# Performance work log

Measured on AMD Instinct MI355X. Metric: run time of the kernel, lower is better.

The kernel has to match this reference:

```python
import jax, jax.numpy as jnp
import numpy as np

N = 200_000           # particles
E = 6_400_000         # neighbor pairs (~32 per particle)
SUPPORT = 0.05
EPS = SUPPORT ** 2 * 0.1
DELTA = 0.1
C0 = 10.0 * float(np.sqrt(2.0 * 9.81 * 0.3))
REST_DENSITY = 1000.0
_KC = 7.0 / float(np.pi)  # 2D Wendland C2 normalization


def kernel_gradient(q, dirs, h):
    # Wendland C2 (2D): W = C/h^2 (1-q)^4 (1+4q), q = r/h in [0,1]
    # dW/dr = C/h^3 * (-20 q (1-q)^3), directed along unit vector dirs
    dkdq = -20.0 * q * (1.0 - q) ** 3 * _KC
    return dirs * (dkdq / h ** 3)[:, None]


def setup_inputs() -> dict:
    key = jax.random.key(0)
    k = jax.random.split(key, 7)
    i = jnp.sort(jax.random.randint(k[0], (E,), 0, N))
    j = jax.random.randint(k[1], (E,), 0, N)
    fluidPosition = jax.random.uniform(k[2], (N, 2), dtype=jnp.float32)
    dx2 = (SUPPORT * 0.5) ** 2
    fluidVolume = dx2 * (1.0 + 0.01 * jax.random.normal(k[3], (N,), dtype=jnp.float32))
    fluidDensity = 0.95 + 0.1 * jax.random.uniform(k[4], (N,), dtype=jnp.float32)
    d = jax.random.normal(k[5], (E, 2), dtype=jnp.float32)
    distances = d / (jnp.linalg.norm(d, axis=1, keepdims=True) + 1e-8)  # unit directions
    radialDistances = jax.random.uniform(k[6], (E,), dtype=jnp.float32, minval=0.05, maxval=1.0)
    return {"fluidPosition": fluidPosition, "fluidVolume": fluidVolume,
            "fluidDensity": fluidDensity, "distances": distances,
            "radialDistances": radialDistances, "i": i, "j": j}


def reference(fluidPosition, fluidVolume, fluidDensity, distances, radialDistances, i, j):
    h = SUPPORT
    n = fluidDensity.shape[0]
    gradW = kernel_gradient(radialDistances, distances, h)          # [E,2]
    r_ba = -distances * (radialDistances * h)[:, None]              # [E,2] displacement
    Vj = fluidVolume[j]

    # --- normalization matrix: sum_j 2 Vj * outer(r_ba, gradW) ---
    term = jnp.einsum('nu,nv->nuv', r_ba, gradW) * (2.0 * Vj)[:, None, None]
    M = jax.ops.segment_sum(term, i, num_segments=n)                # [N,2,2]

    # --- pseudo-inverse + renormalized kernel gradient per edge ---
    Li = jnp.linalg.pinv(M)                                         # [N,2,2]
    grad = jnp.einsum('nuv,nv->nu', Li[i], gradW)                   # [E,2]
    dwij_mag = jnp.sum(jnp.abs(gradW), axis=1)                      # L1 norms
    norm_mag = jnp.sum(jnp.abs(grad), axis=1)
    change = jnp.abs(norm_mag - dwij_mag) / (dwij_mag + 1e-4 * h)
    grad = jnp.where((change < 0.1)[:, None], grad, gradW)

    # --- renormalized density gradient ---
    rho = fluidDensity * REST_DENSITY
    rho_ba = rho[j] - rho[i]
    gradRho = jax.ops.segment_sum((2.0 * rho_ba * Vj)[:, None] * grad, i, num_segments=n)

    # --- deltaSPH density diffusion ---
    rji2 = jnp.sum(r_ba * r_ba, axis=1) + EPS
    densityTerm = 0.5 * jnp.einsum('nu,nu->n', gradRho[i] + gradRho[j], r_ba)
    gradTerm = jnp.einsum('nu,nu->n', gradW, r_ba / rji2[:, None])
    prod = (rho_ba + densityTerm) * gradTerm
    return 2.0 * h * DELTA * C0 * jax.ops.segment_sum(prod * Vj, i, num_segments=n)
```

## Files before the change

kernel.cpp:

```cpp
#include <hip/hip_runtime.h>
#include <hip/hip_fp16.h>
#include <math.h>

#define WAVE   64
#define NPB    32
#define BLOCKT 256
#define SMAX   2

#define KC        2.2281692032865347f
#define H         0.05f
#define INV_H2    400.0f
#define INV_H3    8000.0f
#define EPS_REF   0.00025f
#define K_OUT     0.24261080f
#define REST_RHO  1000.0f

__device__ __forceinline__ float wendland_dkdq(float q) {
    float o = 1.f - q;
    return -20.f * q * o * o * o * KC;
}

union H2F { __half2 h; float f; };
__device__ __forceinline__ float   h2_as_f(__half2 h) { H2F u; u.h = h; return u.f; }
__device__ __forceinline__ __half2 f_as_h2(float f)   { H2F u; u.f = f; return u.h; }

template<int NV>
__device__ __forceinline__ void seg_reduce4(const int k[4], float v[4][NV], float* base) {
    const int lane = threadIdx.x & (WAVE - 1);
    const int k0 = k[0], k3 = k[3];
    const bool split = (k0 != k3);
    const int firstLen  = (k[1]==k0) ? ((k[2]==k0) ? ((k[3]==k0)?4:3) : 2) : 1;
    const int lastStart = (k[2]==k3) ? ((k[1]==k3) ? ((k[0]==k3)?0:1) : 2) : 3;

    float vin[NV], vfirst[NV];
#pragma unroll
    for (int c = 0; c < NV; ++c) {
        float s = v[3][c];
        if (lastStart <= 2) s += v[2][c];
        if (lastStart <= 1) s += v[1][c];
        if (lastStart == 0) s += v[0][c];
        vin[c] = s;
        float f = v[0][c];
        if (firstLen >= 2) f += v[1][c];
        if (firstLen >= 3) f += v[2][c];
        if (firstLen >= 4) f += v[3][c];
        vfirst[c] = f;
    }
#pragma unroll
    for (int idx = 1; idx <= 2; ++idx) {
        if (idx >= firstLen && idx < lastStart && k[idx] >= 0) {
#pragma unroll
            for (int c = 0; c < NV; ++c)
                atomicAdd(base + (size_t)k[idx] * NV + c, v[idx][c]);
        }
    }
    float S[NV];
#pragma unroll
    for (int c = 0; c < NV; ++c) S[c] = vin[c];
    const int klast = k3;
#pragma unroll
    for (int d = 1; d <= 16; d <<= 1) {
        int okey = __shfl_up(klast, d, WAVE);
        float ov[NV];
#pragma unroll
        for (int c = 0; c < NV; ++c) ov[c] = __shfl_up(S[c], d, WAVE);
        if (lane >= d && okey == klast) {
#pragma unroll
            for (int c = 0; c < NV; ++c) S[c] += ov[c];
        }
    }
    const int prevk = __shfl_up(klast, 1, WAVE);
    float P[NV];
#pragma unroll
    for (int c = 0; c < NV; ++c) P[c] = __shfl_up(S[c], 1, WAVE);
    if (split && k0 >= 0) {
        const bool carry = (lane > 0 && prevk == k0);
#pragma unroll
        for (int c = 0; c < NV; ++c)
            atomicAdd(base + (size_t)k0 * NV + c, vfirst[c] + (carry ? P[c] : 0.f));
    }
    const int nk0 = __shfl_down(k0, 1, WAVE);
    const bool tail = (lane == WAVE - 1) || (nk0 != klast);
    if (tail && klast >= 0) {
#pragma unroll
        for (int c = 0; c < NV; ++c)
            atomicAdd(base + (size_t)klast * NV + c, S[c]);
    }
}

struct EW { int jv[4]; float qv[4], dxv[4], dyv[4]; int kv[4]; bool okv[4]; };

__device__ __forceinline__ void load_win(long e0, int beg, int end, int E,
        const int* __restrict__ ej, const float* __restrict__ qarr,
        const float2* __restrict__ dirs, const unsigned char* __restrict__ key8,
        EW& w) {
    if (e0 + 3 < (long)E) {
        int4   j4 = *(const int4*)(ej + e0);
        float4 q4 = *(const float4*)(qarr + e0);
        float4 dA = *(const float4*)((const float*)dirs + 2 * e0);
        float4 dB = *(const float4*)((const float*)dirs + 2 * e0 + 4);
        uchar4 kk = *(const uchar4*)(key8 + e0);
        w.jv[0]=j4.x; w.jv[1]=j4.y; w.jv[2]=j4.z; w.jv[3]=j4.w;
        w.qv[0]=q4.x; w.qv[1]=q4.y; w.qv[2]=q4.z; w.qv[3]=q4.w;
        w.dxv[0]=dA.x; w.dyv[0]=dA.y; w.dxv[1]=dA.z; w.dyv[1]=dA.w;
        w.dxv[2]=dB.x; w.dyv[2]=dB.y; w.dxv[3]=dB.z; w.dyv[3]=dB.w;
        w.kv[0]=kk.x; w.kv[1]=kk.y; w.kv[2]=kk.z; w.kv[3]=kk.w;
    } else {
#pragma unroll
        for (int u = 0; u < 4; ++u) {
            long e = e0 + u;
            if (e < (long)E) {
                w.jv[u] = ej[e]; w.qv[u] = qarr[e]; w.kv[u] = key8[e];
                float2 d = dirs[e]; w.dxv[u] = d.x; w.dyv[u] = d.y;
            } else { w.jv[u]=0; w.qv[u]=0.f; w.dxv[u]=0.f; w.dyv[u]=0.f; w.kv[u]=0; }
        }
    }
#pragma unroll
    for (int u = 0; u < 4; ++u) {
        long e = e0 + u;
        w.okv[u] = (e >= (long)beg) && (e < (long)end);
    }
}

__global__ void k_prep(const int* __restrict__ ei, const float* __restrict__ vol,
                       const float* __restrict__ dens, int* __restrict__ rowptr,
                       float2* __restrict__ vd, unsigned char* __restrict__ key8,
                       int N, int E) {
    int e = blockIdx.x * blockDim.x + threadIdx.x;
    if (e <= E) {
        int prev = (e == 0) ? -1 : ei[e - 1];
        int cur  = (e == E) ? N  : ei[e];
        for (int t = prev + 1; t <= cur; ++t) rowptr[t] = e;
        if (e < E) key8[e] = (unsigned char)(cur & (NPB - 1));
    }
    if (e < N) vd[e] = make_float2(vol[e], dens[e]);
}

__global__ __launch_bounds__(BLOCKT, 4)
void k_AC(const int* __restrict__ ej, const float* __restrict__ qarr,
          const float2* __restrict__ dirs, const float2* __restrict__ vd,
          const int* __restrict__ rowptr, const unsigned char* __restrict__ key8,
          __half2* __restrict__ cst,
          float2* __restrict__ g2, float* __restrict__ outp, int N, int E) {
    __shared__ float  acc6[NPB * 6];
    __shared__ float  Lild[NPB * 3];
    __shared__ float  gld[NPB * 2];
    __shared__ float2 vdl[NPB];
    const int tid = threadIdx.x;
    const int n0  = blockIdx.x * NPB;
    const int nHi = min(n0 + NPB, N);
    if (tid < NPB && n0 + tid < N) vdl[tid] = vd[n0 + tid];
    if (tid < NPB * 6) acc6[tid] = 0.f;
    if (tid < NPB * 2) gld[tid] = 0.f;
    __syncthreads();
    const int  beg = rowptr[n0], end = rowptr[nHi];
    const long beg4 = (long)beg & ~3L;
    const int  waveBase = tid & ~(WAVE - 1);

    int   li_s[4 * SMAX];
    float gwx_s[4 * SMAX], gwy_s[4 * SMAX], val_s[4 * SMAX];
#pragma unroll
    for (int x = 0; x < 4 * SMAX; ++x) { li_s[x] = -1; gwx_s[x]=gwy_s[x]=val_s[x]=0.f; }

#pragma unroll
    for (int c = 0; c < SMAX; ++c) {
        long ebw = beg4 + ((long)c * BLOCKT + waveBase) * 4;
        if (ebw < (long)end) {
            long e0 = beg4 + ((long)c * BLOCKT + tid) * 4;
            EW wd; load_win(e0, beg, end, E, ej, qarr, dirs, key8, wd);
            const bool all4 = wd.okv[0] && wd.okv[1] && wd.okv[2] && wd.okv[3];
            float4 cpack;
            int k[4]; float v[4][6];
#pragma unroll
            for (int u = 0; u < 4; ++u) {
                k[u] = -1;
#pragma unroll
                for (int c2 = 0; c2 < 6; ++c2) v[u][c2] = 0.f;
                if (wd.okv[u]) {
                    int li = wd.kv[u];
                    float q = wd.qv[u], dx = wd.dxv[u], dy = wd.dyv[u];
                    float2 vdj = vd[wd.jv[u]];
                    float wq = wendland_dkdq(q);
                    float t  = q * wq * INV_H2;
                    float s  = -2.f * vdj.x * t;
                    float w2 = wq * INV_H3;
                    float gwx = dx * w2, gwy = dy * w2;
                    float rx = -dx * q * H, ry = -dy * q * H;
                    float rji2 = rx * rx + ry * ry + EPS_REF;
                    float gT = -t / rji2;
                    float gv = gT * vdj.x;
                    float rho_ba = REST_RHO * (vdj.y - vdl[li].y);
                    k[u] = li;
                    v[u][0] = s * dx * dx; v[u][1] = s * dx * dy; v[u][2] = s * dy * dy;
                    v[u][3] = rho_ba * gv; v[u][4] = rx * gv;    v[u][5] = ry * gv;
                    __half2 cp = __floats2half2_rn(0.5f * rx * gv, 0.5f * ry * gv);
                    if (all4) (&cpack.x)[u] = h2_as_f(cp);
                    else      cst[e0 + u] = cp;
                    li_s[c*4+u] = li; gwx_s[c*4+u] = gwx; gwy_s[c*4+u] = gwy;
                    val_s[c*4+u] = 2.f * rho_ba * vdj.x;
                }
            }
            if (all4) ((float4*)cst)[e0 >> 2] = cpack;
            seg_reduce4<6>(k, v, acc6);
        }
    }
    for (int c = SMAX; ; ++c) {
        long ebw = beg4 + ((long)c * BLOCKT + waveBase) * 4;
        if (ebw >= (long)end) break;
        long e0 = beg4 + ((long)c * BLOCKT + tid) * 4;
        EW wd; load_win(e0, beg, end, E, ej, qarr, dirs, key8, wd);
        int k[4]; float v[4][6];
#pragma unroll
        for (int u = 0; u < 4; ++u) {
            k[u] = -1;
#pragma unroll
            for (int c2 = 0; c2 < 6; ++c2) v[u][c2] = 0.f;
            if (wd.okv[u]) {
                int li = wd.kv[u];
                float q = wd.qv[u], dx = wd.dxv[u], dy = wd.dyv[u];
                float2 vdj = vd[wd.jv[u]];
                float wq = wendland_dkdq(q);
                float t  = q * wq * INV_H2;
                float s  = -2.f * vdj.x * t;
                float w2 = wq * INV_H3;
                float gwx = dx * w2, gwy = dy * w2;
                float rx = -dx * q * H, ry = -dy * q * H;
                float rji2 = rx * rx + ry * ry + EPS_REF;
                float gT = -t / rji2;
                float gv = gT * vdj.x;
                float rho_ba = REST_RHO * (vdj.y - vdl[li].y);
                k[u] = li;
                v[u][0] = s * dx * dx; v[u][1] = s * dx * dy; v[u][2] = s * dy * dy;
                v[u][3] = rho_ba * gv; v[u][4] = rx * gv;    v[u][5] = ry * gv;
                cst[e0 + u] = __floats2half2_rn(0.5f * rx * gv, 0.5f * ry * gv);
            }
        }
        seg_reduce4<6>(k, v, acc6);
    }
    __syncthreads();

    if (tid < NPB) {
        float a = acc6[6*tid], b = acc6[6*tid+1], cc = acc6[6*tid+2];
        float half_tr   = 0.5f * (a + cc);
        float half_diff = 0.5f * (a - cc);
        float disc = sqrtf(half_diff * half_diff + b * b);
        float l1 = half_tr + disc, l2 = half_tr - disc;
        float smax = fmaxf(fabsf(l1), fabsf(l2));
        float cutoff = 2.3841858e-6f * smax;
        float i00 = 0.f, i01 = 0.f, i11 = 0.f;
        if (fabsf(l2) > cutoff) {
            float inv = 1.0f / (a * cc - b * b);
            i00 =  cc * inv; i01 = -b * inv; i11 = a * inv;
        } else if (fabsf(l1) > cutoff) {
            float vax = b,       vay = l1 - a;
            float vbx = l1 - cc, vby = b;
            float na = vax*vax + vay*vay, nb = vbx*vbx + vby*vby;
            float vx, vy, n2;
            if (nb >= na) { vx = vbx; vy = vby; n2 = nb; }
            else          { vx = vax; vy = vay; n2 = na; }
            float inv = 1.0f / (l1 * n2);
            i00 = vx*vx*inv; i01 = vx*vy*inv; i11 = vy*vy*inv;
        }
        Lild[3*tid] = i00; Lild[3*tid+1] = i01; Lild[3*tid+2] = i11;
    }
    __syncthreads();

#pragma unroll
    for (int c = 0; c < SMAX; ++c) {
        long ebw = beg4 + ((long)c * BLOCKT + waveBase) * 4;
        if (ebw < (long)end) {
            int k[4]; float v[4][2];
#pragma unroll
            for (int u = 0; u < 4; ++u) {
                int li = li_s[c*4+u];
                k[u] = li; v[u][0] = v[u][1] = 0.f;
                if (li >= 0) {
                    float gwx = gwx_s[c*4+u], gwy = gwy_s[c*4+u];
                    float L0 = Lild[3*li], L1 = Lild[3*li+1], L2v = Lild[3*li+2];
                    float gx = L0 * gwx + L1 * gwy;
                    float gy = L1 * gwx + L2v * gwy;
                    float dm = fabsf(gwx) + fabsf(gwy);
                    float nm = fabsf(gx) + fabsf(gy);
                    float change = fabsf(nm - dm) / (dm + 1e-4f * H);
                    if (!(change < 0.1f)) { gx = gwx; gy = gwy; }
                    v[u][0] = val_s[c*4+u] * gx;
                    v[u][1] = val_s[c*4+u] * gy;
                }
            }
            seg_reduce4<2>(k, v, gld);
        }
    }
    for (int c = SMAX; ; ++c) {
        long ebw = beg4 + ((long)c * BLOCKT + waveBase) * 4;
        if (ebw >= (long)end) break;
        long e0 = beg4 + ((long)c * BLOCKT + tid) * 4;
        EW wd; load_win(e0, beg, end, E, ej, qarr, dirs, key8, wd);
        int k[4]; float v[4][2];
#pragma unroll
        for (int u = 0; u < 4; ++u) {
            k[u] = -1; v[u][0] = v[u][1] = 0.f;
            if (wd.okv[u]) {
                int li = wd.kv[u];
                float q = wd.qv[u], dx = wd.dxv[u], dy = wd.dyv[u];
                float2 vdj = vd[wd.jv[u]];
                float w2 = wendland_dkdq(q) * INV_H3;
                float gwx = dx * w2, gwy = dy * w2;
                float L0 = Lild[3*li], L1 = Lild[3*li+1], L2v = Lild[3*li+2];
                float gx = L0 * gwx + L1 * gwy;
                float gy = L1 * gwx + L2v * gwy;
                float dm = fabsf(gwx) + fabsf(gwy);
                float nm = fabsf(gx) + fabsf(gy);
                float change = fabsf(nm - dm) / (dm + 1e-4f * H);
                if (!(change < 0.1f)) { gx = gwx; gy = gwy; }
                float val = 2.f * REST_RHO * (vdj.y - vdl[li].y) * vdj.x;
                k[u] = li; v[u][0] = val * gx; v[u][1] = val * gy;
            }
        }
        seg_reduce4<2>(k, v, gld);
    }
    __syncthreads();
    if (tid < NPB && n0 + tid < N) {
        float gx = gld[2*tid], gy = gld[2*tid+1];
        g2[n0 + tid]   = make_float2(gx, gy);
        outp[n0 + tid] = acc6[6*tid+3] + 0.5f * (gx * acc6[6*tid+4] + gy * acc6[6*tid+5]);
    }
}

__global__ __launch_bounds__(BLOCKT, 4)
void k_D(const int* __restrict__ ej, const unsigned char* __restrict__ key8,
         const __half2* __restrict__ cst,
         const float2* __restrict__ g2, const float* __restrict__ outp,
         const int* __restrict__ rowptr, float* __restrict__ out, int N, int E) {
    __shared__ float outl[NPB];
    const int tid = threadIdx.x;
    const int n0  = blockIdx.x * NPB;
    const int nHi = min(n0 + NPB, N);
    if (tid < NPB) outl[tid] = 0.f;
    __syncthreads();
    const int  beg = rowptr[n0], end = rowptr[nHi];
    const long beg4 = (long)beg & ~3L;
    const int  waveBase = tid & ~(WAVE - 1);

    for (int c = 0; ; ++c) {
        long ebw = beg4 + ((long)c * BLOCKT + waveBase) * 4;
        if (ebw >= (long)end) break;
        long e0 = beg4 + ((long)c * BLOCKT + tid) * 4;
        int jv[4], kv[4]; float cv[4]; bool okv[4];
        if (e0 + 3 < (long)E) {
            int4   j4 = *(const int4*)(ej + e0);
            float4 c4 = ((const float4*)cst)[e0 >> 2];
            uchar4 kk = *(const uchar4*)(key8 + e0);
            jv[0]=j4.x; jv[1]=j4.y; jv[2]=j4.z; jv[3]=j4.w;
            cv[0]=c4.x; cv[1]=c4.y; cv[2]=c4.z; cv[3]=c4.w;
            kv[0]=kk.x; kv[1]=kk.y; kv[2]=kk.z; kv[3]=kk.w;
        } else {
#pragma unroll
            for (int u = 0; u < 4; ++u) {
                long e = e0 + u;
                if (e < (long)E) { jv[u] = ej[e]; cv[u] = h2_as_f(cst[e]); kv[u] = key8[e]; }
                else             { jv[u] = 0;     cv[u] = 0.f;             kv[u] = 0; }
            }
        }
#pragma unroll
        for (int u = 0; u < 4; ++u) {
            long e = e0 + u;
            okv[u] = (e >= (long)beg) && (e < (long)end);
        }
        float2 gj4[4];
#pragma unroll
        for (int u = 0; u < 4; ++u)
            gj4[u] = okv[u] ? g2[jv[u]] : make_float2(0.f, 0.f);
        int k[4]; float v[4][1];
#pragma unroll
        for (int u = 0; u < 4; ++u) {
            k[u] = -1; v[u][0] = 0.f;
            if (okv[u]) {
                __half2 ch = f_as_h2(cv[u]);
                k[u] = kv[u];
                v[u][0] = gj4[u].x * __low2float(ch) + gj4[u].y * __high2float(ch);
            }
        }
        seg_reduce4<1>(k, v, outl);
    }
    __syncthreads();
    if (tid < NPB && n0 + tid < N)
        out[n0 + tid] = K_OUT * (outp[n0 + tid] + outl[tid]);
}

extern "C" void kernel_launch(void* const* d_in, const int* in_sizes, int n_in,
                              void* d_out, int out_size, void* d_ws, size_t ws_size,
                              hipStream_t stream) {
    const float*  vol  = (const float*)d_in[1];
    const float*  dens = (const float*)d_in[2];
    const float2* dirs = (const float2*)d_in[3];
    const float*  qarr = (const float*)d_in[4];
    const int*    ei   = (const int*)d_in[5];
    const int*    ej   = (const int*)d_in[6];
    const int N = in_sizes[1];
    const int E = in_sizes[4];

    size_t off = 0;
    auto alloc = [&](size_t bytes) { void* r = (char*)d_ws + off;
                                     off = (off + bytes + 15) & ~(size_t)15; return r; };
    int*           rowptr = (int*)          alloc((size_t)(N + 1) * 4);
    float2*        vd     = (float2*)       alloc((size_t)N * 8);
    float2*        g2     = (float2*)       alloc((size_t)N * 8);
    float*         outp   = (float*)        alloc((size_t)N * 4);
    __half2*       cst    = (__half2*)      alloc((size_t)E * 4);
    unsigned char* key8   = (unsigned char*)alloc((size_t)E);
    float*         out    = (float*)d_out;

    const int tb = 256;
    const int gP = (E + 1 + tb - 1) / tb;
    const int gB = (N + NPB - 1) / NPB;

    k_prep<<<gP, tb, 0, stream>>>(ei, vol, dens, rowptr, vd, key8, N, E);
    k_AC  <<<gB, BLOCKT, 0, stream>>>(ej, qarr, dirs, vd, rowptr, key8, cst, g2, outp, N, E);
    k_D   <<<gB, BLOCKT, 0, stream>>>(ej, key8, cst, g2, outp, rowptr, out, N, E);
}
```

Baseline: 243.4 us.

## Restructure final pass as edge-strip segmented reduction with atomic accumulation into output

```diff
diff --git a/kernel.cpp b/kernel.cpp
--- a/kernel.cpp
+++ b/kernel.cpp
@@ -6,6 +6,7 @@
 #define NPB    32
 #define BLOCKT 256
 #define SMAX   2
+#define DSTRIP 1024
 
 #define KC        2.2281692032865347f
 #define H         0.05f
@@ -13,6 +14,7 @@
 #define INV_H3    8000.0f
 #define EPS_REF   0.00025f
 #define K_OUT     0.24261080f
+#define CH_SC     0.12130540f
 #define REST_RHO  1000.0f
 
 __device__ __forceinline__ float wendland_dkdq(float q) {
@@ -141,7 +143,7 @@
           const float2* __restrict__ dirs, const float2* __restrict__ vd,
           const int* __restrict__ rowptr, const unsigned char* __restrict__ key8,
           __half2* __restrict__ cst,
-          float2* __restrict__ g2, float* __restrict__ outp, int N, int E) {
+          float2* __restrict__ g2, float* __restrict__ out, int N, int E) {
     __shared__ float  acc6[NPB * 6];
     __shared__ float  Lild[NPB * 3];
     __shared__ float  gld[NPB * 2];
@@ -193,7 +195,7 @@
                     k[u] = li;
                     v[u][0] = s * dx * dx; v[u][1] = s * dx * dy; v[u][2] = s * dy * dy;
                     v[u][3] = rho_ba * gv; v[u][4] = rx * gv;    v[u][5] = ry * gv;
-                    __half2 cp = __floats2half2_rn(0.5f * rx * gv, 0.5f * ry * gv);
+                    __half2 cp = __floats2half2_rn(CH_SC * rx * gv, CH_SC * ry * gv);
                     if (all4) (&cpack.x)[u] = h2_as_f(cp);
                     else      cst[e0 + u] = cp;
                     li_s[c*4+u] = li; gwx_s[c*4+u] = gwx; gwy_s[c*4+u] = gwy;
@@ -232,7 +234,7 @@
                 k[u] = li;
                 v[u][0] = s * dx * dx; v[u][1] = s * dx * dy; v[u][2] = s * dy * dy;
                 v[u][3] = rho_ba * gv; v[u][4] = rx * gv;    v[u][5] = ry * gv;
-                cst[e0 + u] = __floats2half2_rn(0.5f * rx * gv, 0.5f * ry * gv);
+                cst[e0 + u] = __floats2half2_rn(CH_SC * rx * gv, CH_SC * ry * gv);
             }
         }
         seg_reduce4<6>(k, v, acc6);
@@ -321,70 +323,58 @@
     __syncthreads();
     if (tid < NPB && n0 + tid < N) {
         float gx = gld[2*tid], gy = gld[2*tid+1];
-        g2[n0 + tid]   = make_float2(gx, gy);
-        outp[n0 + tid] = acc6[6*tid+3] + 0.5f * (gx * acc6[6*tid+4] + gy * acc6[6*tid+5]);
+        g2[n0 + tid] = make_float2(gx, gy);
+        out[n0 + tid] = K_OUT * (acc6[6*tid+3]
+                        + 0.5f * (gx * acc6[6*tid+4] + gy * acc6[6*tid+5]));
     }
 }
 
 __global__ __launch_bounds__(BLOCKT, 4)
-void k_D(const int* __restrict__ ej, const unsigned char* __restrict__ key8,
-         const __half2* __restrict__ cst,
-         const float2* __restrict__ g2, const float* __restrict__ outp,
-         const int* __restrict__ rowptr, float* __restrict__ out, int N, int E) {
-    __shared__ float outl[NPB];
-    const int tid = threadIdx.x;
-    const int n0  = blockIdx.x * NPB;
-    const int nHi = min(n0 + NPB, N);
-    if (tid < NPB) outl[tid] = 0.f;
-    __syncthreads();
-    const int  beg = rowptr[n0], end = rowptr[nHi];
-    const long beg4 = (long)beg & ~3L;
-    const int  waveBase = tid & ~(WAVE - 1);
-
-    for (int c = 0; ; ++c) {
-        long ebw = beg4 + ((long)c * BLOCKT + waveBase) * 4;
-        if (ebw >= (long)end) break;
-        long e0 = beg4 + ((long)c * BLOCKT + tid) * 4;
-        int jv[4], kv[4]; float cv[4]; bool okv[4];
+void k_D(const int* __restrict__ ei, const int* __restrict__ ej,
+         const __half2* __restrict__ cst, const float2* __restrict__ g2,
+         float* __restrict__ out, int E) {
+    const int lane = threadIdx.x & (WAVE - 1);
+    const int wid  = blockIdx.x * (BLOCKT / WAVE) + (threadIdx.x >> 6);
+    const long s0  = (long)wid * DSTRIP;
+    if (s0 >= (long)E) return;
+
+    int   ik[4][4]; int jk[4][4]; float ck[4][4];
+#pragma unroll
+    for (int c = 0; c < 4; ++c) {
+        long e0 = s0 + (long)c * 256 + (long)lane * 4;
         if (e0 + 3 < (long)E) {
+            int4   i4 = *(const int4*)(ei + e0);
             int4   j4 = *(const int4*)(ej + e0);
             float4 c4 = ((const float4*)cst)[e0 >> 2];
-            uchar4 kk = *(const uchar4*)(key8 + e0);
-            jv[0]=j4.x; jv[1]=j4.y; jv[2]=j4.z; jv[3]=j4.w;
-            cv[0]=c4.x; cv[1]=c4.y; cv[2]=c4.z; cv[3]=c4.w;
-            kv[0]=kk.x; kv[1]=kk.y; kv[2]=kk.z; kv[3]=kk.w;
+            ik[c][0]=i4.x; ik[c][1]=i4.y; ik[c][2]=i4.z; ik[c][3]=i4.w;
+            jk[c][0]=j4.x; jk[c][1]=j4.y; jk[c][2]=j4.z; jk[c][3]=j4.w;
+            ck[c][0]=c4.x; ck[c][1]=c4.y; ck[c][2]=c4.z; ck[c][3]=c4.w;
         } else {
 #pragma unroll
             for (int u = 0; u < 4; ++u) {
                 long e = e0 + u;
-                if (e < (long)E) { jv[u] = ej[e]; cv[u] = h2_as_f(cst[e]); kv[u] = key8[e]; }
-                else             { jv[u] = 0;     cv[u] = 0.f;             kv[u] = 0; }
+                if (e < (long)E) { ik[c][u] = ei[e]; jk[c][u] = ej[e]; ck[c][u] = h2_as_f(cst[e]); }
+                else             { ik[c][u] = -1;    jk[c][u] = 0;     ck[c][u] = 0.f; }
             }
         }
+    }
+    float2 gj[4][4];
+#pragma unroll
+    for (int c = 0; c < 4; ++c)
+#pragma unroll
+        for (int u = 0; u < 4; ++u)
+            gj[c][u] = (ik[c][u] >= 0) ? g2[jk[c][u]] : make_float2(0.f, 0.f);
+#pragma unroll
+    for (int c = 0; c < 4; ++c) {
+        int k[4]; float v[4][1];
 #pragma unroll
         for (int u = 0; u < 4; ++u) {
-            long e = e0 + u;
-            okv[u] = (e >= (long)beg) && (e < (long)end);
-        }
-        float2 gj4[4];
-#pragma unroll
-        for (int u = 0; u < 4; ++u)
-            gj4[u] = okv[u] ? g2[jv[u]] : make_float2(0.f, 0.f);
-        int k[4]; float v[4][1];
-#pragma unroll
-        for (int u = 0; u < 4; ++u) {
-            k[u] = -1; v[u][0] = 0.f;
-            if (okv[u]) {
-                __half2 ch = f_as_h2(cv[u]);
-                k[u] = kv[u];
-                v[u][0] = gj4[u].x * __low2float(ch) + gj4[u].y * __high2float(ch);
-            }
-        }
-        seg_reduce4<1>(k, v, outl);
-    }
-    __syncthreads();
-    if (tid < NPB && n0 + tid < N)
-        out[n0 + tid] = K_OUT * (outp[n0 + tid] + outl[tid]);
+            k[u] = ik[c][u];
+            __half2 ch = f_as_h2(ck[c][u]);
+            v[u][0] = gj[c][u].x * __low2float(ch) + gj[c][u].y * __high2float(ch);
+        }
+        seg_reduce4<1>(k, v, out);
+    }
 }
 
 extern "C" void kernel_launch(void* const* d_in, const int* in_sizes, int n_in,
@@ -405,7 +395,6 @@
     int*           rowptr = (int*)          alloc((size_t)(N + 1) * 4);
     float2*        vd     = (float2*)       alloc((size_t)N * 8);
     float2*        g2     = (float2*)       alloc((size_t)N * 8);
-    float*         outp   = (float*)        alloc((size_t)N * 4);
     __half2*       cst    = (__half2*)      alloc((size_t)E * 4);
     unsigned char* key8   = (unsigned char*)alloc((size_t)E);
     float*         out    = (float*)d_out;
@@ -413,8 +402,10 @@
     const int tb = 256;
     const int gP = (E + 1 + tb - 1) / tb;
     const int gB = (N + NPB - 1) / NPB;
+    const int nWaves = (E + DSTRIP - 1) / DSTRIP;
+    const int gD = (nWaves + (BLOCKT / WAVE) - 1) / (BLOCKT / WAVE);
 
     k_prep<<<gP, tb, 0, stream>>>(ei, vol, dens, rowptr, vd, key8, N, E);
-    k_AC  <<<gB, BLOCKT, 0, stream>>>(ej, qarr, dirs, vd, rowptr, key8, cst, g2, outp, N, E);
-    k_D   <<<gB, BLOCKT, 0, stream>>>(ej, key8, cst, g2, outp, rowptr, out, N, E);
-}
+    k_AC  <<<gB, BLOCKT, 0, stream>>>(ej, qarr, dirs, vd, rowptr, key8, cst, g2, out, N, E);
+    k_D   <<<gD, BLOCKT, 0, stream>>>(ei, ej, cst, g2, out, E);
+}
```

After: 251.2 us. 1.03x slower.
